# Optimization experiments

Hardware: AMD Instinct MI355X
Metric: run time of the kernel (lower is better)

## Reference

```python
import jax, jax.numpy as jnp
import numpy as np

B, S, D, H, DFF = 4, 2048, 1024, 16, 4096
DH = D // H  # per-head query/value dim
EPS = 1e-5


def layer_norm(x, scale, bias):
    mu = jnp.mean(x, axis=-1, keepdims=True)
    var = jnp.mean(jnp.square(x - mu), axis=-1, keepdims=True)
    return (x - mu) * jax.lax.rsqrt(var + EPS) * scale + bias


def setup_inputs() -> dict:
    key = jax.random.key(0)
    ks = jax.random.split(key, 16)
    s_in = 1.0 / np.sqrt(D)
    s_ff = 1.0 / np.sqrt(DFF)
    inp = {
        "x": jax.random.normal(ks[0], (B, S, D), jnp.float32),
        # per-head Q/K/V projections stacked along head axis [H, D, DH]
        "wq": jax.random.normal(ks[1], (H, D, DH), jnp.float32) * s_in,
        "bq": jax.random.normal(ks[2], (H, DH), jnp.float32) * 0.01,
        "wk": jax.random.normal(ks[3], (H, D, DH), jnp.float32) * s_in,
        "bk": jax.random.normal(ks[4], (H, DH), jnp.float32) * 0.01,
        "wv": jax.random.normal(ks[5], (H, D, DH), jnp.float32) * s_in,
        "bv": jax.random.normal(ks[6], (H, DH), jnp.float32) * 0.01,
        "wo": jax.random.normal(ks[7], (H * DH, D), jnp.float32) * s_in,
        "bo": jax.random.normal(ks[8], (D,), jnp.float32) * 0.01,
        "ln1_s": jnp.ones((D,), jnp.float32),
        "ln1_b": jnp.zeros((D,), jnp.float32),
        "w1": jax.random.normal(ks[9], (D, DFF), jnp.float32) * s_in,
        "b1": jax.random.normal(ks[10], (DFF,), jnp.float32) * 0.01,
        "w2": jax.random.normal(ks[11], (DFF, D), jnp.float32) * s_ff,
        "b2": jax.random.normal(ks[12], (D,), jnp.float32) * 0.01,
        "ln2_s": jnp.ones((D,), jnp.float32),
        "ln2_b": jnp.zeros((D,), jnp.float32),
    }
    return inp


def reference(x, wq, bq, wk, bk, wv, bv, wo, bo, ln1_s, ln1_b, w1, b1, w2, b2, ln2_s, ln2_b):
    # --- masked multi-head self-attention (all heads vectorized) ---
    q = jnp.einsum('bsd,hde->bhse', x, wq) + bq[None, :, None, :]  # [B,H,S,DH]
    k = jnp.einsum('bsd,hde->bhse', x, wk) + bk[None, :, None, :]
    v = jnp.einsum('bsd,hde->bhse', x, wv) + bv[None, :, None, :]
    scores = jnp.einsum('bhse,bhte->bhst', q, k)  # [B,H,S,S]
    causal = jnp.tril(jnp.ones((S, S), bool))  # mask sets strict upper triangle to -inf
    scores = jnp.where(causal, scores, -jnp.inf)
    scale = jnp.float32(DH) ** 0.5
    attn = jax.nn.softmax(scores / scale, axis=-1)
    out = jnp.einsum('bhst,bhte->bhse', attn, v)  # [B,H,S,DH]
    concat = out.transpose(0, 2, 1, 3).reshape(B, S, H * DH)
    attn_out = concat @ wo + bo
    y = layer_norm(x + attn_out, ln1_s, ln1_b)  # post-LN residual (dropout=0)
    # --- feed-forward ---
    ff = jax.nn.relu(y @ w1 + b1) @ w2 + b2
    return layer_norm(y + ff, ln2_s, ln2_b)
```

## Files before the change

kernel.cpp:

```cpp
#include <hip/hip_runtime.h>
#include <hip/hip_bf16.h>
#include <cstdint>

#define BB 4
#define SS 2048
#define DD 1024
#define HH 16
#define DHH 64
#define DFFN 4096
#define MROWS (BB*SS)

typedef __attribute__((ext_vector_type(8))) __bf16 v8bf;
typedef __attribute__((ext_vector_type(4))) float v4f;

static __device__ __forceinline__ unsigned short f2bf(float f) {
  unsigned u = __float_as_uint(f);
  u = (u + 0x7fffu + ((u >> 16) & 1u)) >> 16;
  return (unsigned short)u;
}

static __device__ __forceinline__ void mfma16(v4f& d, v8bf a, v8bf b) {
  d = __builtin_amdgcn_mfma_f32_16x16x32_bf16(a, b, d, 0, 0, 0);
}

static __device__ __forceinline__ void gload16(const void* g, void* l) {
  __builtin_amdgcn_global_load_lds(
      (const __attribute__((address_space(1))) unsigned int*)(unsigned long long)g,
      (__attribute__((address_space(3))) unsigned int*)(unsigned int)(unsigned long long)l,
      16, 0, 0);
}


__global__ __launch_bounds__(256) void pack_x_k(const float* __restrict__ x,
                                                unsigned short* __restrict__ xb) {
  int i = blockIdx.x * 256 + threadIdx.x;
  float4 v = ((const float4*)x)[i];
  ushort4 o;
  o.x = f2bf(v.x); o.y = f2bf(v.y); o.z = f2bf(v.z); o.w = f2bf(v.w);
  ((ushort4*)xb)[i] = o;
}

static __device__ __forceinline__ void transpose_tile(const float* __restrict__ src,
                                                      unsigned short* __restrict__ dst,
                                                      int R, int C, int rt, int ct) {
  __shared__ float tile[32][33];
  const int tx = threadIdx.x, ty = threadIdx.y;
  #pragma unroll
  for (int j = 0; j < 4; ++j)
    tile[ty + j * 8][tx] = src[(size_t)(rt + ty + j * 8) * C + ct + tx];
  __syncthreads();
  #pragma unroll
  for (int j = 0; j < 4; ++j)
    dst[(size_t)(ct + ty + j * 8) * R + rt + tx] = f2bf(tile[tx][ty + j * 8]);
}

__global__ __launch_bounds__(256) void transpose_k(const float* __restrict__ src,
                                                   unsigned short* __restrict__ dst,
                                                   int R, int C) {
  transpose_tile(src, dst, R, C, blockIdx.y * 32, blockIdx.x * 32);
}

__global__ __launch_bounds__(256) void transpose_qkv_k(const float* __restrict__ wq,
                                                       const float* __restrict__ wk,
                                                       const float* __restrict__ wv,
                                                       unsigned short* __restrict__ dst) {
  const int z = blockIdx.z;
  const int w = z >> 4, h = z & 15;
  const float* src = (w == 0) ? wq : ((w == 1) ? wk : wv);
  src += (size_t)h * DD * DHH;
  unsigned short* d = dst + (size_t)(w * DD + h * DHH) * DD;
  transpose_tile(src, d, DD, DHH, blockIdx.y * 32, blockIdx.x * 32);
}


template<int MODE>
__global__ __launch_bounds__(512, 2) void gemm_bt(
    const unsigned short* __restrict__ A, const unsigned short* __restrict__ Bt,
    const float* __restrict__ bias0, const float* __restrict__ bias1,
    const float* __restrict__ bias2,
    float* __restrict__ outF, unsigned short* __restrict__ o0,
    unsigned short* __restrict__ o1, unsigned short* __restrict__ o2,
    int M, int N, int K) {
  extern __shared__ __align__(16) char smem[];
  const int tid = threadIdx.x;
  const int wid = tid >> 6, lane = tid & 63;
  const int l15 = lane & 15, kg = lane >> 4;
  const int m0 = blockIdx.y * 256, n0 = blockIdx.x * 256;
  const int wm = (wid >> 2) * 128, wn = (wid & 3) * 64;

  const int sr8 = wid * 8 + (lane >> 3);
  const int sge = ((lane & 7) ^ ((lane >> 3) & 7)) << 3;
  const int swr = (l15 & 7) << 4;

  const int NK = K >> 6;
  v4f acc[8][4] = {};
  v8bf bf_[4][2];

  #define STA(q, kt, lb) gload16(A  + (size_t)(m0 + (q) * 64 + sr8) * K + (kt) * 64 + sge, \
                                 (lb) + (q) * 8192 + wid * 1024)
  #define STB(q, kt, lb) gload16(Bt + (size_t)(n0 + (q) * 64 + sr8) * K + (kt) * 64 + sge, \
                                 (lb) + (q) * 8192 + wid * 1024)

  {
    char* A0b = smem;
    char* B0b = smem + 65536;
    STB(0, 0, B0b); STB(1, 0, B0b); STB(2, 0, B0b); STB(3, 0, B0b);
    STA(0, 0, A0b); STA(2, 0, A0b); STA(1, 0, A0b); STA(3, 0, A0b);
  }

  #pragma unroll 1
  for (int j = 0; j < NK; ++j) {
    char* Ac = smem + (j & 1) * 32768;
    char* Bc = smem + 65536 + (j & 1) * 32768;
    char* An = smem + ((j + 1) & 1) * 32768;
    char* Bn = smem + 65536 + ((j + 1) & 1) * 32768;
    const bool more = (j + 1 < NK);

    #pragma unroll
    for (int p = 0; p < 4; ++p) {
      if (more) {
        if (p == 0)      { STB(0, j + 1, Bn); STB(1, j + 1, Bn); }
        else if (p == 1) { STB(2, j + 1, Bn); STB(3, j + 1, Bn); }
        else if (p == 2) { STA(0, j + 1, An); STA(2, j + 1, An); }
        else             { STA(1, j + 1, An); STA(3, j + 1, An); }
      }
      if (p == 0) {
        if (more) asm volatile("s_waitcnt vmcnt(4)" ::: "memory");
        else      asm volatile("s_waitcnt vmcnt(2)" ::: "memory");
      } else if (p == 2) {
        if (more) asm volatile("s_waitcnt vmcnt(6)" ::: "memory");
        else      asm volatile("s_waitcnt vmcnt(0)" ::: "memory");
      }
      __builtin_amdgcn_s_barrier();

      if (p == 0) {
        #pragma unroll
        for (int nr = 0; nr < 4; ++nr)
          #pragma unroll
          for (int ks = 0; ks < 2; ++ks)
            bf_[nr][ks] = *(const v8bf*)(Bc + (wn + nr * 16 + l15) * 128 +
                                         (((ks * 4 + kg) << 4) ^ swr));
      }
      v8bf af[2][2];
      #pragma unroll
      for (int mi = 0; mi < 2; ++mi)
        #pragma unroll
        for (int ks = 0; ks < 2; ++ks)
          af[mi][ks] = *(const v8bf*)(Ac + (wm + (2 * p + mi) * 16 + l15) * 128 +
                                      (((ks * 4 + kg) << 4) ^ swr));
      asm volatile("s_waitcnt lgkmcnt(0)" ::: "memory");
      __builtin_amdgcn_sched_barrier(0);

      __builtin_amdgcn_s_setprio(1);
      #pragma unroll
      for (int mi = 0; mi < 2; ++mi)
        #pragma unroll
        for (int nr = 0; nr < 4; ++nr)
          #pragma unroll
          for (int ks = 0; ks < 2; ++ks)
            mfma16(acc[2 * p + mi][nr], af[mi][ks], bf_[nr][ks]);
      __builtin_amdgcn_s_setprio(0);
      __builtin_amdgcn_s_barrier();
    }
  }
  #undef STA
  #undef STB

  #pragma unroll
  for (int nr = 0; nr < 4; ++nr) {
    const int col = n0 + wn + nr * 16 + l15;
    #pragma unroll
    for (int mr = 0; mr < 8; ++mr) {
      const int rb = m0 + wm + mr * 16 + kg * 4;
      if constexpr (MODE == 0) {
        const int seg = col >> 10, cc = col & 1023;
        const int h = cc >> 6, e = cc & 63;
        const float bias = (seg == 0) ? bias0[cc] : (seg == 1) ? bias1[cc] : bias2[cc];
        if (seg < 2) {
          unsigned short* dst = (seg == 0) ? o0 : o1;
          const float scl = (seg == 0) ? 0.125f : 1.0f;
          #pragma unroll
          for (int i = 0; i < 4; ++i) {
            const int row = rb + i, b = row >> 11, s = row & (SS - 1);
            dst[(((size_t)b * HH + h) * SS + s) * DHH + e] =
                f2bf((acc[mr][nr][i] + bias) * scl);
          }
        } else {
          const int b = rb >> 11, s0q = rb & (SS - 1);
          ushort4 pv;
          pv.x = f2bf(acc[mr][nr][0] + bias);
          pv.y = f2bf(acc[mr][nr][1] + bias);
          pv.z = f2bf(acc[mr][nr][2] + bias);
          pv.w = f2bf(acc[mr][nr][3] + bias);
          *(ushort4*)&o2[(((size_t)b * HH + h) * DHH + e) * SS + s0q] = pv;
        }
      } else if constexpr (MODE == 1 || MODE == 3) {
        const float bias = bias0[col];
        #pragma unroll
        for (int i = 0; i < 4; ++i)
          outF[(size_t)(rb + i) * N + col] = acc[mr][nr][i] + bias;
      } else {
        const float bias = bias0[col];
        #pragma unroll
        for (int i = 0; i < 4; ++i)
          o0[(size_t)(rb + i) * N + col] = f2bf(fmaxf(acc[mr][nr][i] + bias, 0.f));
      }
    }
  }
}

__global__ __launch_bounds__(256) void attn_k(const unsigned short* __restrict__ q,
                                              const unsigned short* __restrict__ k,
                                              const unsigned short* __restrict__ vt,
                                              unsigned short* __restrict__ concat) {
  __shared__ __align__(16) unsigned short Ks[64 * 64];
  __shared__ __align__(16) unsigned short Vs[64 * 64];
  __shared__ __align__(16) unsigned short PL[4][32 * 72];

  const int tid = threadIdx.x, wid = tid >> 6, lane = tid & 63;
  const int l15 = lane & 15, kg = lane >> 4;
  const int bh = blockIdx.y, b = bh >> 4, h = bh & 15;

  const char* kb = (const char*)(k + (size_t)bh * SS * DHH);
  const char* vb = (const char*)(vt + (size_t)bh * DHH * SS);
  unsigned short* ob = concat + (size_t)b * SS * DD + h * DHH;

  const int srow = wid * 16 + (lane >> 3);
  const int swz_c = ((lane & 7) * 16) ^ ((lane >> 3) << 4);
  const int swr = (l15 & 7) << 4;
  unsigned short* pl = &PL[wid][0];

  #pragma unroll 1
  for (int half = 0; half < 2; ++half) {
    const int qt = (half == 0) ? (int)blockIdx.x : 15 - (int)blockIdx.x;
    const int q0 = qt * 128;
    const int q0w = q0 + wid * 32;
    const unsigned short* qb = q + ((size_t)bh * SS + q0w) * DHH;

    v8bf qf[2][2];
    #pragma unroll
    for (int n = 0; n < 2; ++n)
      #pragma unroll
      for (int ks = 0; ks < 2; ++ks)
        qf[n][ks] = *(const v8bf*)&qb[(n * 16 + l15) * DHH + ks * 32 + kg * 8];

    v4f acc[4][2] = {};
    float mrun[2] = {-1e30f, -1e30f}, ssum[2] = {0.f, 0.f};

    const int T = q0 / 64 + 2;
    for (int it = 0; it < T; ++it) {
      const int t0 = it * 64;
      #pragma unroll
      for (int iss = 0; iss < 2; ++iss) {
        const int r = srow + iss * 8;
        gload16(kb + (size_t)(t0 + r) * 128 + swz_c, &Ks[(wid * 16 + iss * 8) * 64]);
        gload16(vb + (size_t)r * 4096 + (size_t)t0 * 2 + swz_c, &Vs[(wid * 16 + iss * 8) * 64]);
      }
      __syncthreads();

      if (t0 <= q0w + 31) {
        v4f sT[4][2] = {};
        #pragma unroll
        for (int mt = 0; mt < 4; ++mt) {
          #pragma unroll
          for (int ks = 0; ks < 2; ++ks) {
            const v8bf kf = *(const v8bf*)((const char*)Ks + (mt * 16 + l15) * 128 +
                                           ((ks * 64 + kg * 16) ^ swr));
            mfma16(sT[mt][0], kf, qf[0][ks]);
            mfma16(sT[mt][1], kf, qf[1][ks]);
          }
        }

        #pragma unroll
        for (int n = 0; n < 2; ++n) {
          const int qrow = q0w + n * 16 + l15;
          const bool full = (t0 + 63 <= q0w + n * 16);
          float p[16];
          float mx = -1e30f;
          #pragma unroll
          for (int mt = 0; mt < 4; ++mt)
            #pragma unroll
            for (int rg = 0; rg < 4; ++rg) {
              float s = sT[mt][n][rg];
              if (!full) s = (t0 + mt * 16 + kg * 4 + rg <= qrow) ? s : -1e30f;
              p[mt * 4 + rg] = s;
              mx = fmaxf(mx, s);
            }
          mx = fmaxf(mx, __shfl_xor(mx, 16));
          mx = fmaxf(mx, __shfl_xor(mx, 32));
          const float mnew = fmaxf(mrun[n], mx);
          const float fac = __expf(mrun[n] - mnew);
          mrun[n] = mnew;
          float ts = 0.f;
          #pragma unroll
          for (int i = 0; i < 16; ++i) { p[i] = __expf(p[i] - mnew); ts += p[i]; }
          ts += __shfl_xor(ts, 16);
          ts += __shfl_xor(ts, 32);
          ssum[n] = ssum[n] * fac + ts;
          #pragma unroll
          for (int mt = 0; mt < 4; ++mt) acc[mt][n] *= fac;
          #pragma unroll
          for (int mt = 0; mt < 4; ++mt) {
            uint2 w;
            w.x = (unsigned)f2bf(p[mt * 4 + 0]) | ((unsigned)f2bf(p[mt * 4 + 1]) << 16);
            w.y = (unsigned)f2bf(p[mt * 4 + 2]) | ((unsigned)f2bf(p[mt * 4 + 3]) << 16);
            *(uint2*)((char*)pl + (n * 16 + l15) * 144 + mt * 32 + kg * 8) = w;
          }
        }
        asm volatile("s_waitcnt lgkmcnt(0)" ::: "memory");
        __builtin_amdgcn_sched_barrier(0);

        #pragma unroll
        for (int ks = 0; ks < 2; ++ks) {
          v8bf pb[2];
          #pragma unroll
          for (int nt = 0; nt < 2; ++nt)
            pb[nt] = *(const v8bf*)((const char*)pl + (nt * 16 + l15) * 144 + ks * 64 + kg * 16);
          #pragma unroll
          for (int mt = 0; mt < 4; ++mt) {
            const v8bf va = *(const v8bf*)((const char*)Vs + (mt * 16 + l15) * 128 +
                                           ((ks * 64 + kg * 16) ^ swr));
            mfma16(acc[mt][0], va, pb[0]);
            mfma16(acc[mt][1], va, pb[1]);
          }
        }
      }
      __syncthreads();
    }

    const float inv[2] = {1.0f / ssum[0], 1.0f / ssum[1]};
    #pragma unroll
    for (int nt = 0; nt < 2; ++nt) {
      const int qrow = q0w + nt * 16 + l15;
      #pragma unroll
      for (int mt = 0; mt < 4; ++mt) {
        ushort4 o4;
        o4.x = f2bf(acc[mt][nt][0] * inv[nt]);
        o4.y = f2bf(acc[mt][nt][1] * inv[nt]);
        o4.z = f2bf(acc[mt][nt][2] * inv[nt]);
        o4.w = f2bf(acc[mt][nt][3] * inv[nt]);
        *(ushort4*)&ob[(size_t)qrow * DD + mt * 16 + kg * 4] = o4;
      }
    }
  }
}

template<bool WB>
__global__ __launch_bounds__(256) void resid_ln_k(const float* __restrict__ a,
                                                  const float* __restrict__ t,
                                                  const float* __restrict__ sc,
                                                  const float* __restrict__ bi,
                                                  float* __restrict__ yo,
                                                  unsigned short* __restrict__ yb) {
  __shared__ float rs[4], rs2[4];
  const int row = blockIdx.x, tid = threadIdx.x;
  const int wid = tid >> 6, lane = tid & 63;
  const float4 x4 = ((const float4*)(a + (size_t)row * DD))[tid];
  const float4 t4 = ((const float4*)(t + (size_t)row * DD))[tid];
  const float v0 = x4.x + t4.x, v1 = x4.y + t4.y, v2 = x4.z + t4.z, v3 = x4.w + t4.w;
  float s = v0 + v1 + v2 + v3;
  float s2 = v0 * v0 + v1 * v1 + v2 * v2 + v3 * v3;
  #pragma unroll
  for (int m = 1; m < 64; m <<= 1) { s += __shfl_xor(s, m); s2 += __shfl_xor(s2, m); }
  if (lane == 0) { rs[wid] = s; rs2[wid] = s2; }
  __syncthreads();
  s = rs[0] + rs[1] + rs[2] + rs[3];
  s2 = rs2[0] + rs2[1] + rs2[2] + rs2[3];
  const float mu = s * (1.0f / DD);
  const float var = s2 * (1.0f / DD) - mu * mu;
  const float rstd = rsqrtf(var + 1e-5f);
  const int c0 = tid * 4;
  const float o0 = (v0 - mu) * rstd * sc[c0 + 0] + bi[c0 + 0];
  const float o1 = (v1 - mu) * rstd * sc[c0 + 1] + bi[c0 + 1];
  const float o2 = (v2 - mu) * rstd * sc[c0 + 2] + bi[c0 + 2];
  const float o3 = (v3 - mu) * rstd * sc[c0 + 3] + bi[c0 + 3];
  float4 ov; ov.x = o0; ov.y = o1; ov.z = o2; ov.w = o3;
  ((float4*)(yo + (size_t)row * DD))[tid] = ov;
  if (WB) {
    ushort4 ub; ub.x = f2bf(o0); ub.y = f2bf(o1); ub.z = f2bf(o2); ub.w = f2bf(o3);
    ((ushort4*)(yb + (size_t)row * DD))[tid] = ub;
  }
}


extern "C" void kernel_launch(void* const* d_in, const int* in_sizes, int n_in,
                              void* d_out, int out_size, void* d_ws, size_t ws_size,
                              hipStream_t stream) {
  const float* x   = (const float*)d_in[0];
  const float* wq  = (const float*)d_in[1];
  const float* bq  = (const float*)d_in[2];
  const float* wk  = (const float*)d_in[3];
  const float* bk  = (const float*)d_in[4];
  const float* wv  = (const float*)d_in[5];
  const float* bv  = (const float*)d_in[6];
  const float* wo  = (const float*)d_in[7];
  const float* bo  = (const float*)d_in[8];
  const float* l1s = (const float*)d_in[9];
  const float* l1b = (const float*)d_in[10];
  const float* w1  = (const float*)d_in[11];
  const float* b1  = (const float*)d_in[12];
  const float* w2  = (const float*)d_in[13];
  const float* b2  = (const float*)d_in[14];
  const float* l2s = (const float*)d_in[15];
  const float* l2b = (const float*)d_in[16];

  char* ws = (char*)d_ws;
  unsigned short* WO_T  = (unsigned short*)(ws + 0);
  unsigned short* W1_T  = (unsigned short*)(ws + 2097152);
  unsigned short* W2_T  = (unsigned short*)(ws + 10485760);
  float*          Y     = (float*)(ws + 18874368);
  unsigned short* YBF   = (unsigned short*)(ws + 52428800);
  float*          TMP1  = (float*)(ws + 69206016);
  unsigned short* XBF   = (unsigned short*)(ws + 102760448);
  unsigned short* WQKVT = (unsigned short*)(ws + 119537664);
  unsigned short* QB    = (unsigned short*)(ws + 125829120);
  unsigned short* KB    = (unsigned short*)(ws + 142606336);
  unsigned short* VTB   = (unsigned short*)(ws + 159383552);
  unsigned short* CONC  = (unsigned short*)(ws + 176160768);
  unsigned short* H1    = (unsigned short*)(ws + 102760448);
  float*          TMP2  = TMP1;

  constexpr int GSMEM = 131072;
  hipFuncSetAttribute(reinterpret_cast<const void*>(gemm_bt<0>),
                      hipFuncAttributeMaxDynamicSharedMemorySize, GSMEM);
  hipFuncSetAttribute(reinterpret_cast<const void*>(gemm_bt<1>),
                      hipFuncAttributeMaxDynamicSharedMemorySize, GSMEM);
  hipFuncSetAttribute(reinterpret_cast<const void*>(gemm_bt<2>),
                      hipFuncAttributeMaxDynamicSharedMemorySize, GSMEM);
  hipFuncSetAttribute(reinterpret_cast<const void*>(gemm_bt<3>),
                      hipFuncAttributeMaxDynamicSharedMemorySize, GSMEM);

  pack_x_k<<<8192, 256, 0, stream>>>(x, XBF);
  transpose_qkv_k<<<dim3(2, 32, 48), dim3(32, 8), 0, stream>>>(wq, wk, wv, WQKVT);
  transpose_k<<<dim3(32, 32),  dim3(32, 8), 0, stream>>>(wo, WO_T, 1024, 1024);
  transpose_k<<<dim3(128, 32), dim3(32, 8), 0, stream>>>(w1, W1_T, 1024, 4096);
  transpose_k<<<dim3(32, 128), dim3(32, 8), 0, stream>>>(w2, W2_T, 4096, 1024);

  gemm_bt<0><<<dim3(12, 32), 512, GSMEM, stream>>>(XBF, WQKVT, bq, bk, bv,
      nullptr, QB, KB, VTB, MROWS, 3072, 1024);
  attn_k<<<dim3(8, 64), 256, 0, stream>>>(QB, KB, VTB, CONC);
  gemm_bt<1><<<dim3(4, 32), 512, GSMEM, stream>>>(CONC, WO_T, bo, nullptr, nullptr,
      TMP1, nullptr, nullptr, nullptr, MROWS, 1024, 1024);
  resid_ln_k<true><<<8192, 256, 0, stream>>>(x, TMP1, l1s, l1b, Y, YBF);
  gemm_bt<2><<<dim3(16, 32), 512, GSMEM, stream>>>(YBF, W1_T, b1, nullptr, nullptr,
      nullptr, H1, nullptr, nullptr, MROWS, 4096, 1024);
  gemm_bt<3><<<dim3(4, 32), 512, GSMEM, stream>>>(H1, W2_T, b2, nullptr, nullptr,
      TMP2, nullptr, nullptr, nullptr, MROWS, 1024, 4096);
  resid_ln_k<false><<<8192, 256, 0, stream>>>(Y, TMP2, l2s, l2b, (float*)d_out, nullptr);
}
```

Baseline: 470.3 us.

## Restructure GEMM K-loop to batch LDS fragment loads and reschedule prefetch waits

Restructures the GEMM main loop. Each K-step now loads all B fragments and half of the A fragments from shared memory up front, then the second half mid-iteration, instead of doing per-quarter A loads each followed by an lgkmcnt(0) wait. Global prefetches for the next tile are issued in two groups, and the vmcnt waits and barriers are rearranged so MFMA work overlaps outstanding loads. This aims to cut LDS wait stalls and barrier overhead, at the cost of more live registers for the fragments, which may hurt occupancy or cause spills.

```diff
diff --git a/kernel.cpp b/kernel.cpp
--- a/kernel.cpp
+++ b/kernel.cpp
@@ -94,7 +94,6 @@
 
   const int NK = K >> 6;
   v4f acc[8][4] = {};
-  v8bf bf_[4][2];
 
   #define STA(q, kt, lb) gload16(A  + (size_t)(m0 + (q) * 64 + sr8) * K + (kt) * 64 + sge, \
                                  (lb) + (q) * 8192 + wid * 1024)
@@ -106,6 +105,8 @@
     char* B0b = smem + 65536;
     STB(0, 0, B0b); STB(1, 0, B0b); STB(2, 0, B0b); STB(3, 0, B0b);
     STA(0, 0, A0b); STA(2, 0, A0b); STA(1, 0, A0b); STA(3, 0, A0b);
+    asm volatile("s_waitcnt vmcnt(2)" ::: "memory");
+    __builtin_amdgcn_s_barrier();
   }
 
   #pragma unroll 1
@@ -116,52 +117,77 @@
     char* Bn = smem + 65536 + ((j + 1) & 1) * 32768;
     const bool more = (j + 1 < NK);
 
-    #pragma unroll
-    for (int p = 0; p < 4; ++p) {
-      if (more) {
-        if (p == 0)      { STB(0, j + 1, Bn); STB(1, j + 1, Bn); }
-        else if (p == 1) { STB(2, j + 1, Bn); STB(3, j + 1, Bn); }
-        else if (p == 2) { STA(0, j + 1, An); STA(2, j + 1, An); }
-        else             { STA(1, j + 1, An); STA(3, j + 1, An); }
-      }
-      if (p == 0) {
-        if (more) asm volatile("s_waitcnt vmcnt(4)" ::: "memory");
-        else      asm volatile("s_waitcnt vmcnt(2)" ::: "memory");
-      } else if (p == 2) {
-        if (more) asm volatile("s_waitcnt vmcnt(6)" ::: "memory");
-        else      asm volatile("s_waitcnt vmcnt(0)" ::: "memory");
-      }
-      __builtin_amdgcn_s_barrier();
-
-      if (p == 0) {
-        #pragma unroll
-        for (int nr = 0; nr < 4; ++nr)
-          #pragma unroll
-          for (int ks = 0; ks < 2; ++ks)
-            bf_[nr][ks] = *(const v8bf*)(Bc + (wn + nr * 16 + l15) * 128 +
-                                         (((ks * 4 + kg) << 4) ^ swr));
-      }
-      v8bf af[2][2];
-      #pragma unroll
-      for (int mi = 0; mi < 2; ++mi)
+    v8bf bf_[4][2], af01[4][2];
+    #pragma unroll
+    for (int nr = 0; nr < 4; ++nr)
+      #pragma unroll
+      for (int ks = 0; ks < 2; ++ks)
+        bf_[nr][ks] = *(const v8bf*)(Bc + (wn + nr * 16 + l15) * 128 +
+                                     (((ks * 4 + kg) << 4) ^ swr));
+    #pragma unroll
+    for (int mi = 0; mi < 4; ++mi)
+      #pragma unroll
+      for (int ks = 0; ks < 2; ++ks)
+        af01[mi][ks] = *(const v8bf*)(Ac + (wm + mi * 16 + l15) * 128 +
+                                      (((ks * 4 + kg) << 4) ^ swr));
+    if (more) { STB(0, j + 1, Bn); STB(1, j + 1, Bn); STB(2, j + 1, Bn); STB(3, j + 1, Bn); }
+    __builtin_amdgcn_s_setprio(1);
+    #pragma unroll
+    for (int mi = 0; mi < 2; ++mi)
+      #pragma unroll
+      for (int nr = 0; nr < 4; ++nr)
         #pragma unroll
         for (int ks = 0; ks < 2; ++ks)
-          af[mi][ks] = *(const v8bf*)(Ac + (wm + (2 * p + mi) * 16 + l15) * 128 +
+          mfma16(acc[mi][nr], af01[mi][ks], bf_[nr][ks]);
+    __builtin_amdgcn_s_setprio(0);
+    __builtin_amdgcn_s_barrier();
+
+    if (more) {
+      STA(0, j + 1, An); STA(2, j + 1, An); STA(1, j + 1, An); STA(3, j + 1, An);
+      asm volatile("s_waitcnt vmcnt(8)" ::: "memory");
+    } else {
+      asm volatile("s_waitcnt vmcnt(0)" ::: "memory");
+    }
+    __builtin_amdgcn_s_setprio(1);
+    #pragma unroll
+    for (int mi = 2; mi < 4; ++mi)
+      #pragma unroll
+      for (int nr = 0; nr < 4; ++nr)
+        #pragma unroll
+        for (int ks = 0; ks < 2; ++ks)
+          mfma16(acc[mi][nr], af01[mi][ks], bf_[nr][ks]);
+    __builtin_amdgcn_s_setprio(0);
+    __builtin_amdgcn_s_barrier();
+
+    v8bf af23[4][2];
+    #pragma unroll
+    for (int mi = 0; mi < 4; ++mi)
+      #pragma unroll
+      for (int ks = 0; ks < 2; ++ks)
+        af23[mi][ks] = *(const v8bf*)(Ac + (wm + (mi + 4) * 16 + l15) * 128 +
                                       (((ks * 4 + kg) << 4) ^ swr));
-      asm volatile("s_waitcnt lgkmcnt(0)" ::: "memory");
-      __builtin_amdgcn_sched_barrier(0);
-
-      __builtin_amdgcn_s_setprio(1);
-      #pragma unroll
-      for (int mi = 0; mi < 2; ++mi)
-        #pragma unroll
-        for (int nr = 0; nr < 4; ++nr)
-          #pragma unroll
-          for (int ks = 0; ks < 2; ++ks)
-            mfma16(acc[2 * p + mi][nr], af[mi][ks], bf_[nr][ks]);
-      __builtin_amdgcn_s_setprio(0);
-      __builtin_amdgcn_s_barrier();
-    }
+    __builtin_amdgcn_s_setprio(1);
+    #pragma unroll
+    for (int mi = 0; mi < 2; ++mi)
+      #pragma unroll
+      for (int nr = 0; nr < 4; ++nr)
+        #pragma unroll
+        for (int ks = 0; ks < 2; ++ks)
+          mfma16(acc[mi + 4][nr], af23[mi][ks], bf_[nr][ks]);
+    __builtin_amdgcn_s_setprio(0);
+    __builtin_amdgcn_s_barrier();
+
+    if (more) asm volatile("s_waitcnt vmcnt(2)" ::: "memory");
+    __builtin_amdgcn_s_setprio(1);
+    #pragma unroll
+    for (int mi = 2; mi < 4; ++mi)
+      #pragma unroll
+      for (int nr = 0; nr < 4; ++nr)
+        #pragma unroll
+        for (int ks = 0; ks < 2; ++ks)
+          mfma16(acc[mi + 4][nr], af23[mi][ks], bf_[nr][ks]);
+    __builtin_amdgcn_s_setprio(0);
+    __builtin_amdgcn_s_barrier();
   }
   #undef STA
   #undef STB
```

After: 448.8 us. 4.6% less time.
